# Kernel optimization log

Hardware: AMD Instinct MI355X
Metric: run time of the kernel (lower is better)

The kernel has to match this reference:

```python
import jax, jax.numpy as jnp
import numpy as np

# SplineConv (PyG), dim=1, kernel_size=2, degree=1, open spline, aggr='mean',
# root_weight=True, bias=True.
# For K=2, m=1, dim=1 the B-spline basis per edge reduces exactly to
#   basis = (1 - u, u) with kernel indices (0, 1), u = edge_attr[:, 0] in [0, 1].

N_NODES = 50000
N_EDGES = 1600000
D_IN = 128
D_OUT = 128


def setup_inputs() -> dict:
    key = jax.random.key(0)
    k1, k2, k3, k4, k5, k6, k7 = jax.random.split(key, 7)
    x = jax.random.normal(k1, (N_NODES, D_IN), dtype=jnp.float32)
    edge_index = jax.random.randint(k2, (2, N_EDGES), 0, N_NODES, dtype=jnp.int64)
    edge_attr = jax.random.uniform(k3, (N_EDGES, 1), dtype=jnp.float32)
    # Glorot-ish init for spline weights [K^dim=2, D_IN, D_OUT]
    scale = 1.0 / np.sqrt(D_IN)
    W = jax.random.normal(k4, (2, D_IN, D_OUT), dtype=jnp.float32) * scale
    W_root = jax.random.normal(k5, (D_IN, D_OUT), dtype=jnp.float32) * scale
    bias = jax.random.normal(k6, (D_OUT,), dtype=jnp.float32) * 0.01
    return {"x": x, "edge_index": edge_index, "edge_attr": edge_attr,
            "W": W, "W_root": W_root, "bias": bias}


def reference(x, edge_index, edge_attr, W, W_root, bias):
    n = x.shape[0]
    src, dst = edge_index[0], edge_index[1]
    u = jnp.clip(edge_attr[:, 0], 0.0, 1.0)          # [E]
    # Node-level GEMMs for both kernel weight slots (cheaper than per-edge GEMM)
    h = jnp.einsum('nd,kde->kne', x, W)              # [2, N, D_OUT]
    # Per-edge spline-weighted message: (1-u)*h0[src] + u*h1[src]
    msg = (1.0 - u)[:, None] * h[0][src] + u[:, None] * h[1][src]  # [E, D_OUT]
    agg = jax.ops.segment_sum(msg, dst, num_segments=n)            # [N, D_OUT]
    deg = jax.ops.segment_sum(jnp.ones_like(u), dst, num_segments=n)
    agg = agg / jnp.maximum(deg, 1.0)[:, None]       # mean aggregation
    return agg + x @ W_root + bias
```

## Files before the change

kernel.cpp:

```cpp
#include <hip/hip_runtime.h>

static constexpr int N = 50000;
static constexpr int E = 1600000;
static constexpr int D = 128;
static constexpr int NB = (N + 63) / 64;
static constexpr int BIN_BLKS = 256;
static constexpr int CHUNK = E / BIN_BLKS;
static constexpr int SLOTS = (CHUNK + 1023) / 1024;
static constexpr int BKT_CAP = 3072;
static constexpr int CVT_BLKS = (N * D / 8 + 1023) / 1024;
static constexpr int W_BLKS = 48;

typedef __attribute__((ext_vector_type(8))) short short8;
typedef __attribute__((ext_vector_type(4))) float f32x4;
typedef __attribute__((ext_vector_type(2))) float f32x2;

__device__ __forceinline__ uint bf16rne2(float a, float b) {
    uint ua = __float_as_uint(a), ub = __float_as_uint(b);
    ua += 0x7fffu + ((ua >> 16) & 1u);
    ub += 0x7fffu + ((ub >> 16) & 1u);
    return (ua >> 16) | (ub & 0xffff0000u);
}

__device__ __forceinline__ void gload16(const void* g, void* l) {
    __builtin_amdgcn_global_load_lds(
        (const __attribute__((address_space(1))) void*)g,
        (__attribute__((address_space(3))) void*)l, 16, 0, 0);
}

__device__ __forceinline__ int logical_blk() {
    return (blockIdx.x & 7) * (BIN_BLKS / 8) + (blockIdx.x >> 3);
}

__global__ __launch_bounds__(1024) void binprep_k(
        const int* __restrict__ ei, const float* __restrict__ ea,
        const float* __restrict__ x, const float* __restrict__ W,
        const float* __restrict__ Wr, int* __restrict__ gcur,
        uint* __restrict__ pay, ushort* __restrict__ xb,
        uchar* __restrict__ xf8, ushort* __restrict__ Wt) {
    __shared__ int hist[NB];
    __shared__ int base[NB];
    int t = threadIdx.x;
    if (blockIdx.x < BIN_BLKS) {
        int b = logical_blk();
        for (int j = t; j < NB; j += 1024) hist[j] = 0;
        __syncthreads();
        int b0 = b * CHUNK;
        uint mypay[SLOTS];
        int  mybkt[SLOTS];
        int  myrank[SLOTS];
#pragma unroll
        for (int k = 0; k < SLOTS; ++k) {
            int i = b0 + t + k * 1024;
            myrank[k] = -1;
            if (t + k * 1024 < CHUNK) {
                int dst = ei[E + i];
                if ((unsigned)dst < (unsigned)N) {
                    int src = ei[i];
                    float u = fminf(fmaxf(ea[i], 0.0f), 1.0f);
                    uint u10 = (uint)(u * 1023.0f + 0.5f);
                    int bkt = dst >> 6;
                    mybkt[k] = bkt;
                    mypay[k] = (u10 << 22) | ((uint)(dst & 63) << 16) | (uint)src;
                    myrank[k] = atomicAdd(&hist[bkt], 1);
                }
            }
        }
        __syncthreads();
        for (int j = t; j < NB; j += 1024) {
            int c = hist[j];
            base[j] = c ? atomicAdd(&gcur[j], c) : 0;
        }
        __syncthreads();
#pragma unroll
        for (int k = 0; k < SLOTS; ++k) {
            if (myrank[k] >= 0) {
                int pos = base[mybkt[k]] + myrank[k];
                if (pos < BKT_CAP)
                    pay[(size_t)mybkt[k] * BKT_CAP + pos] = mypay[k];
            }
        }
    } else if (blockIdx.x < BIN_BLKS + CVT_BLKS) {
        int i = (blockIdx.x - BIN_BLKS) * 1024 + t;
        if (i < N * D / 8) {
            float4 v0 = ((const float4*)x)[2 * i];
            float4 v1 = ((const float4*)x)[2 * i + 1];
            uint4 ob = { bf16rne2(v0.x, v0.y), bf16rne2(v0.z, v0.w),
                         bf16rne2(v1.x, v1.y), bf16rne2(v1.z, v1.w) };
            ((uint4*)xb)[i] = ob;
            int lo = __builtin_amdgcn_cvt_pk_fp8_f32(v0.x, v0.y, 0, false);
            lo = __builtin_amdgcn_cvt_pk_fp8_f32(v0.z, v0.w, lo, true);
            int hi = __builtin_amdgcn_cvt_pk_fp8_f32(v1.x, v1.y, 0, false);
            hi = __builtin_amdgcn_cvt_pk_fp8_f32(v1.z, v1.w, hi, true);
            uint2 o8 = { (uint)lo, (uint)hi };
            ((uint2*)xf8)[i] = o8;
        }
    } else {
        int i = (blockIdx.x - BIN_BLKS - CVT_BLKS) * 1024 + t;
        int n = i / 384, r = i % 384;
        float v = (r < 256) ? W[(size_t)r * 128 + n]
                            : Wr[(size_t)(r - 256) * 128 + n];
        uint u = __float_as_uint(v);
        u += 0x7fffu + ((u >> 16) & 1u);
        Wt[(size_t)n * 384 + r] = (ushort)(u >> 16);
    }
}

__global__ __launch_bounds__(1024) void sortagg_k(
        const uchar* __restrict__ xf8, const int* __restrict__ gcur,
        const uint* __restrict__ pay, ushort* __restrict__ a0b,
        ushort* __restrict__ a1b) {
    __shared__ uint srt[BKT_CAP];
    __shared__ int hist[64];
    __shared__ int off64[65];
    int b = blockIdx.x, t = threadIdx.x;
    int beg = b * BKT_CAP;
    int c = gcur[b];
    if (c > BKT_CAP) c = BKT_CAP;
    if (t < 64) hist[t] = 0;
    __syncthreads();
    uint mypay[3]; int myrank[3];
#pragma unroll
    for (int k = 0; k < 3; ++k) {
        int i = t + k * 1024;
        if (i < c) {
            uint p = pay[beg + i];
            mypay[k] = p;
            myrank[k] = atomicAdd(&hist[(p >> 16) & 63], 1);
        }
    }
    __syncthreads();
    if (t < 64) {
        int v = hist[t];
        int s = v;
        for (int d = 1; d < 64; d <<= 1) {
            int o = __shfl_up(s, d);
            if (t >= d) s += o;
        }
        off64[t] = s - v;
        if (t == 63) off64[64] = s;
    }
    __syncthreads();
#pragma unroll
    for (int k = 0; k < 3; ++k) {
        int i = t + k * 1024;
        if (i < c) {
            uint p = mypay[k];
            srt[off64[(p >> 16) & 63] + myrank[k]] = p;
        }
    }
    __syncthreads();

    int lane = t & 63;
    int wv   = t >> 6;
    int grp  = (lane >> 4);
    int cl   = lane & 15;
    int nloc = wv * 4 + grp;
    int s0 = off64[nloc], s1 = off64[nloc + 1];
    int deg = s1 - s0;

    f32x2 S[4], T[4];
#pragma unroll
    for (int q = 0; q < 4; ++q) { S[q] = 0.f; T[q] = 0.f; }

    int j = s0;
    for (; j + 3 < s1; j += 4) {
        uint p[4];
        uint2 v[4];
#pragma unroll
        for (int d = 0; d < 4; ++d) p[d] = srt[j + d];
#pragma unroll
        for (int d = 0; d < 4; ++d)
            v[d] = *(const uint2*)(xf8 + (size_t)(p[d] & 0xffffu) * D + cl * 8);
#pragma unroll
        for (int d = 0; d < 4; ++d) {
            float u = (float)(p[d] >> 22) * (1.0f / 1023.0f);
            f32x2 u2 = {u, u};
            f32x2 xv0 = __builtin_amdgcn_cvt_pk_f32_fp8((int)v[d].x, false);
            f32x2 xv1 = __builtin_amdgcn_cvt_pk_f32_fp8((int)v[d].x, true);
            f32x2 xv2 = __builtin_amdgcn_cvt_pk_f32_fp8((int)v[d].y, false);
            f32x2 xv3 = __builtin_amdgcn_cvt_pk_f32_fp8((int)v[d].y, true);
            S[0] += xv0; T[0] = u2 * xv0 + T[0];
            S[1] += xv1; T[1] = u2 * xv1 + T[1];
            S[2] += xv2; T[2] = u2 * xv2 + T[2];
            S[3] += xv3; T[3] = u2 * xv3 + T[3];
        }
    }
    for (; j < s1; ++j) {
        uint p0 = srt[j];
        uint2 v0 = *(const uint2*)(xf8 + (size_t)(p0 & 0xffffu) * D + cl * 8);
        float u = (float)(p0 >> 22) * (1.0f / 1023.0f);
        f32x2 u2 = {u, u};
        f32x2 xv0 = __builtin_amdgcn_cvt_pk_f32_fp8((int)v0.x, false);
        f32x2 xv1 = __builtin_amdgcn_cvt_pk_f32_fp8((int)v0.x, true);
        f32x2 xv2 = __builtin_amdgcn_cvt_pk_f32_fp8((int)v0.y, false);
        f32x2 xv3 = __builtin_amdgcn_cvt_pk_f32_fp8((int)v0.y, true);
        S[0] += xv0; T[0] = u2 * xv0 + T[0];
        S[1] += xv1; T[1] = u2 * xv1 + T[1];
        S[2] += xv2; T[2] = u2 * xv2 + T[2];
        S[3] += xv3; T[3] = u2 * xv3 + T[3];
    }

    int node = b * 64 + nloc;
    if (node < N) {
        float inv = 1.0f / fmaxf((float)deg, 1.0f);
        uint4 oa = { bf16rne2((S[0].x - T[0].x) * inv, (S[0].y - T[0].y) * inv),
                     bf16rne2((S[1].x - T[1].x) * inv, (S[1].y - T[1].y) * inv),
                     bf16rne2((S[2].x - T[2].x) * inv, (S[2].y - T[2].y) * inv),
                     bf16rne2((S[3].x - T[3].x) * inv, (S[3].y - T[3].y) * inv) };
        uint4 ob = { bf16rne2(T[0].x * inv, T[0].y * inv),
                     bf16rne2(T[1].x * inv, T[1].y * inv),
                     bf16rne2(T[2].x * inv, T[2].y * inv),
                     bf16rne2(T[3].x * inv, T[3].y * inv) };
        *(uint4*)(a0b + (size_t)node * D + cl * 8) = oa;
        *(uint4*)(a1b + (size_t)node * D + cl * 8) = ob;
    }
}

__global__ __launch_bounds__(256) void gemm_k(
        const ushort* __restrict__ a0b, const ushort* __restrict__ a1b,
        const ushort* __restrict__ xb, const ushort* __restrict__ Wt,
        const float* __restrict__ bias, float* __restrict__ out) {
    __shared__ ushort As[128 * 64];
    __shared__ ushort Bs[128 * 64];

    int t    = threadIdx.x;
    int lane = t & 63;
    int w    = t >> 6;
    int r2   = w >> 1, c2 = w & 1;
    int q    = lane >> 4;
    int l16  = lane & 15;
    int row0 = blockIdx.x * 128;
    int rsub  = lane >> 3;
    int cslot = lane & 7;
    int xorc  = cslot ^ rsub;

    f32x4 acc[4][4];
#pragma unroll
    for (int i = 0; i < 4; ++i)
#pragma unroll
        for (int j = 0; j < 4; ++j) acc[i][j] = 0.f;

    const ushort* Asrc[3] = {a0b, a1b, xb};

#pragma unroll
    for (int kt = 0; kt < 384; kt += 64) {
        const ushort* Ab = Asrc[kt >> 7];
        int ko = kt & 127;
#pragma unroll
        for (int h = 0; h < 4; ++h) {
            int region = h * 4 + w;
            int r = region * 8 + rsub;
            int ra = row0 + r; ra = ra < N ? ra : N - 1;
            gload16(Ab + (size_t)ra * 128 + ko + xorc * 8, As + region * 512);
            gload16(Wt + (size_t)r * 384 + kt + xorc * 8,  Bs + region * 512);
        }
        __syncthreads();
#pragma unroll
        for (int kk = 0; kk < 2; ++kk) {
            short8 af[4], bf[4];
#pragma unroll
            for (int mt = 0; mt < 4; ++mt) {
                int r = r2 * 64 + mt * 16 + l16;
                int slot = (kk * 4 + q) ^ (r & 7);
                af[mt] = *(const short8*)&As[r * 64 + slot * 8];
            }
#pragma unroll
            for (int nt = 0; nt < 4; ++nt) {
                int n = c2 * 64 + nt * 16 + l16;
                int slot = (kk * 4 + q) ^ (n & 7);
                bf[nt] = *(const short8*)&Bs[n * 64 + slot * 8];
            }
#pragma unroll
            for (int mt = 0; mt < 4; ++mt)
#pragma unroll
                for (int nt = 0; nt < 4; ++nt)
                    acc[mt][nt] = __builtin_amdgcn_mfma_f32_16x16x32_bf16(
                        af[mt], bf[nt], acc[mt][nt], 0, 0, 0);
        }
        __syncthreads();
    }

#pragma unroll
    for (int nt = 0; nt < 4; ++nt) {
        int col = c2 * 64 + nt * 16 + l16;
        float bb = bias[col];
#pragma unroll
        for (int mt = 0; mt < 4; ++mt) {
#pragma unroll
            for (int r = 0; r < 4; ++r) {
                int row = row0 + r2 * 64 + mt * 16 + q * 4 + r;
                if (row < N) out[(size_t)row * 128 + col] = acc[mt][nt][r] + bb;
            }
        }
    }
}

extern "C" void kernel_launch(void* const* d_in, const int* in_sizes, int n_in,
                              void* d_out, int out_size, void* d_ws, size_t ws_size,
                              hipStream_t stream) {
    const float* x    = (const float*)d_in[0];
    const int*   ei   = (const int*)d_in[1];
    const float* ea   = (const float*)d_in[2];
    const float* W    = (const float*)d_in[3];
    const float* Wr   = (const float*)d_in[4];
    const float* bias = (const float*)d_in[5];
    float* out = (float*)d_out;

    char* ws = (char*)d_ws;
    size_t o = 0;
    auto alloc = [&](size_t bytes) -> void* {
        void* p = ws + o;
        o = (o + bytes + 255) & ~(size_t)255;
        return p;
    };
    int*    gcur = (int*)alloc((size_t)NB * 4);
    uint*   pay  = (uint*)alloc((size_t)NB * BKT_CAP * 4);
    ushort* xb   = (ushort*)alloc((size_t)N * D * 2);
    uchar*  xf8  = (uchar*)alloc((size_t)N * D);
    ushort* a0b  = (ushort*)alloc((size_t)N * D * 2);
    ushort* a1b  = (ushort*)alloc((size_t)N * D * 2);
    ushort* Wt   = (ushort*)alloc((size_t)128 * 384 * 2);
    (void)ws_size; (void)in_sizes; (void)n_in; (void)out_size;

    hipMemsetAsync(gcur, 0, (size_t)NB * 4, stream);
    binprep_k<<<BIN_BLKS + CVT_BLKS + W_BLKS, 1024, 0, stream>>>(
                 ei, ea, x, W, Wr, gcur, pay, xb, xf8, Wt);
    sortagg_k<<<NB, 1024, 0, stream>>>(xf8, gcur, pay, a0b, a1b);
    gemm_k   <<<(N + 127) / 128, 256, 0, stream>>>(a0b, a1b, xb, Wt, bias, out);
}
```

Before: 161.2 us.

## Sort binned edges in LDS before scatter; load GEMM operands directly from global

```diff
diff --git a/kernel.cpp b/kernel.cpp
--- a/kernel.cpp
+++ b/kernel.cpp
@@ -22,12 +22,6 @@
     return (ua >> 16) | (ub & 0xffff0000u);
 }
 
-__device__ __forceinline__ void gload16(const void* g, void* l) {
-    __builtin_amdgcn_global_load_lds(
-        (const __attribute__((address_space(1))) void*)g,
-        (__attribute__((address_space(3))) void*)l, 16, 0, 0);
-}
-
 __device__ __forceinline__ int logical_blk() {
     return (blockIdx.x & 7) * (BIN_BLKS / 8) + (blockIdx.x >> 3);
 }
@@ -39,11 +33,17 @@
         uint* __restrict__ pay, ushort* __restrict__ xb,
         uchar* __restrict__ xf8, ushort* __restrict__ Wt) {
     __shared__ int hist[NB];
+    __shared__ int pfx[NB];
     __shared__ int base[NB];
+    __shared__ uint srtpay[CHUNK];
+    __shared__ int  srtpos[CHUNK];
+    __shared__ int wsum[16];
+    __shared__ int tot_s;
     int t = threadIdx.x;
+    int lane = t & 63, wv = t >> 6;
     if (blockIdx.x < BIN_BLKS) {
         int b = logical_blk();
-        for (int j = t; j < NB; j += 1024) hist[j] = 0;
+        if (t < NB) hist[t] = 0;
         __syncthreads();
         int b0 = b * CHUNK;
         uint mypay[SLOTS];
@@ -67,18 +67,48 @@
             }
         }
         __syncthreads();
-        for (int j = t; j < NB; j += 1024) {
-            int c = hist[j];
-            base[j] = c ? atomicAdd(&gcur[j], c) : 0;
+        int c = (t < NB) ? hist[t] : 0;
+        int s = c;
+#pragma unroll
+        for (int d = 1; d < 64; d <<= 1) {
+            int o = __shfl_up(s, d);
+            if (lane >= d) s += o;
+        }
+        if (lane == 63) wsum[wv] = s;
+        __syncthreads();
+        if (t < 16) {
+            int v = wsum[t];
+            int si = v;
+#pragma unroll
+            for (int d = 1; d < 16; d <<= 1) {
+                int o = __shfl_up(si, d);
+                if (t >= d) si += o;
+            }
+            wsum[t] = si - v;
+            if (t == 15) tot_s = si;
+        }
+        __syncthreads();
+        int excl = s - c + wsum[wv];
+        if (t < NB) {
+            pfx[t] = excl;
+            base[t] = c ? atomicAdd(&gcur[t], c) : 0;
         }
         __syncthreads();
 #pragma unroll
         for (int k = 0; k < SLOTS; ++k) {
             if (myrank[k] >= 0) {
-                int pos = base[mybkt[k]] + myrank[k];
-                if (pos < BKT_CAP)
-                    pay[(size_t)mybkt[k] * BKT_CAP + pos] = mypay[k];
+                int bk = mybkt[k];
+                int slot = pfx[bk] + myrank[k];
+                srtpay[slot] = mypay[k];
+                int p = base[bk] + myrank[k];
+                srtpos[slot] = (p < BKT_CAP) ? (bk * BKT_CAP + p) : -1;
             }
+        }
+        __syncthreads();
+        int tot = tot_s;
+        for (int i = t; i < tot; i += 1024) {
+            int pos = srtpos[i];
+            if (pos >= 0) pay[pos] = srtpay[i];
         }
     } else if (blockIdx.x < BIN_BLKS + CVT_BLKS) {
         int i = (blockIdx.x - BIN_BLKS) * 1024 + t;
@@ -221,9 +251,6 @@
         const ushort* __restrict__ a0b, const ushort* __restrict__ a1b,
         const ushort* __restrict__ xb, const ushort* __restrict__ Wt,
         const float* __restrict__ bias, float* __restrict__ out) {
-    __shared__ ushort As[128 * 64];
-    __shared__ ushort Bs[128 * 64];
-
     int t    = threadIdx.x;
     int lane = t & 63;
     int w    = t >> 6;
@@ -231,9 +258,6 @@
     int q    = lane >> 4;
     int l16  = lane & 15;
     int row0 = blockIdx.x * 128;
-    int rsub  = lane >> 3;
-    int cslot = lane & 7;
-    int xorc  = cslot ^ rsub;
 
     f32x4 acc[4][4];
 #pragma unroll
@@ -243,42 +267,32 @@
 
     const ushort* Asrc[3] = {a0b, a1b, xb};
 
-#pragma unroll
-    for (int kt = 0; kt < 384; kt += 64) {
+    int arow[4];
+#pragma unroll
+    for (int mt = 0; mt < 4; ++mt) {
+        int r = row0 + r2 * 64 + mt * 16 + l16;
+        arow[mt] = r < N ? r : N - 1;
+    }
+
+#pragma unroll
+    for (int kt = 0; kt < 384; kt += 32) {
         const ushort* Ab = Asrc[kt >> 7];
-        int ko = kt & 127;
-#pragma unroll
-        for (int h = 0; h < 4; ++h) {
-            int region = h * 4 + w;
-            int r = region * 8 + rsub;
-            int ra = row0 + r; ra = ra < N ? ra : N - 1;
-            gload16(Ab + (size_t)ra * 128 + ko + xorc * 8, As + region * 512);
-            gload16(Wt + (size_t)r * 384 + kt + xorc * 8,  Bs + region * 512);
-        }
-        __syncthreads();
-#pragma unroll
-        for (int kk = 0; kk < 2; ++kk) {
-            short8 af[4], bf[4];
-#pragma unroll
-            for (int mt = 0; mt < 4; ++mt) {
-                int r = r2 * 64 + mt * 16 + l16;
-                int slot = (kk * 4 + q) ^ (r & 7);
-                af[mt] = *(const short8*)&As[r * 64 + slot * 8];
-            }
-#pragma unroll
-            for (int nt = 0; nt < 4; ++nt) {
-                int n = c2 * 64 + nt * 16 + l16;
-                int slot = (kk * 4 + q) ^ (n & 7);
-                bf[nt] = *(const short8*)&Bs[n * 64 + slot * 8];
-            }
-#pragma unroll
-            for (int mt = 0; mt < 4; ++mt)
-#pragma unroll
-                for (int nt = 0; nt < 4; ++nt)
-                    acc[mt][nt] = __builtin_amdgcn_mfma_f32_16x16x32_bf16(
-                        af[mt], bf[nt], acc[mt][nt], 0, 0, 0);
-        }
-        __syncthreads();
+        int ko = (kt & 127) + q * 8;
+        short8 af[4], bf[4];
+#pragma unroll
+        for (int mt = 0; mt < 4; ++mt)
+            af[mt] = *(const short8*)(Ab + (size_t)arow[mt] * 128 + ko);
+#pragma unroll
+        for (int nt = 0; nt < 4; ++nt) {
+            int n = c2 * 64 + nt * 16 + l16;
+            bf[nt] = *(const short8*)(Wt + (size_t)n * 384 + kt + q * 8);
+        }
+#pragma unroll
+        for (int mt = 0; mt < 4; ++mt)
+#pragma unroll
+            for (int nt = 0; nt < 4; ++nt)
+                acc[mt][nt] = __builtin_amdgcn_mfma_f32_16x16x32_bf16(
+                    af[mt], bf[nt], acc[mt][nt], 0, 0, 0);
     }
 
 #pragma unroll
```

Result: slower. 171.2 us (+6.2%).
